# Optimization experiments

Hardware: AMD Instinct MI355X
Metric: run time of the kernel (lower is better)

The kernel has to match this reference:

```python
import jax, jax.numpy as jnp
import numpy as np

BETA = 0.25  # commitment_cost


def setup_inputs() -> dict:
    key = jax.random.key(0)
    k1, k2 = jax.random.split(key)
    N, K, D = 32768, 8192, 512
    z = jax.random.normal(k1, (N, D), dtype=jnp.float32)
    # mimic nn.init.uniform_(codebook, -1/K, 1/K)
    codebook = jax.random.uniform(k2, (K, D), dtype=jnp.float32,
                                  minval=-1.0 / K, maxval=1.0 / K)
    return {"z": z, "codebook": codebook}


def reference(z, codebook):
    # squared L2 distances: ||z||^2 + ||c||^2 - 2 z c^T   -> [N, K]
    d = (jnp.sum(z * z, axis=1, keepdims=True)
         + jnp.sum(codebook * codebook, axis=1)
         - 2.0 * (z @ codebook.T))
    indices = jnp.argmin(d, axis=1)            # [N] int
    z_q = codebook[indices]                    # [N, D] gather (grad flows to codebook)
    # commit_loss = beta * mse(z.detach(), z_q)
    commit_loss = BETA * jnp.mean((jax.lax.stop_gradient(z) - z_q) ** 2)
    # straight-through estimator
    z_st = z + jax.lax.stop_gradient(z_q - z)
    return z_st, indices, commit_loss
```

## Files before the change

kernel.cpp:

```cpp
#include <hip/hip_runtime.h>
#include <cfloat>
#include <cstdint>
#include <cstddef>

#define N_ROWS 32768
#define K_CODES 8192
#define DIM 512
#define BETA 0.25

typedef unsigned short u16;
typedef _Float16 half8 __attribute__((ext_vector_type(8)));
typedef float f32x4 __attribute__((ext_vector_type(4)));

#define BKH 64
#define OVCAP 512
#define DELTA_A 0.4f

#define GLOAD_LDS16(g, l)                                          \
  __builtin_amdgcn_global_load_lds(                                \
      (const __attribute__((address_space(1))) void*)(g),          \
      (__attribute__((address_space(3))) void*)(l), 16, 0, 0)

__device__ inline u16 f2h(float x) {
  union { _Float16 h; u16 u; } c;
  c.h = (_Float16)x;
  return c.u;
}

__global__ __launch_bounds__(256)
void vq_zprep(const float* __restrict__ z, u16* __restrict__ zh,
              float* __restrict__ s1out, int* __restrict__ ovcnt) {
  if (blockIdx.x == 0 && threadIdx.x == 0) *ovcnt = 0;
  const int wv = threadIdx.x >> 6;
  const int lane = threadIdx.x & 63;
  const int half = lane >> 5;
  const int g = (lane >> 3) & 3;
  const int j = lane & 7;
  const int row = blockIdx.x * 8 + wv * 2 + half;
  const float* p = z + (size_t)row * DIM + g * 128 + j;
  u16* q = zh + (size_t)row * DIM + g * 128 + j;
  float x = p[0];
  q[0] = f2h(x);
  float r = __fmul_rn(x, x);
#pragma unroll
  for (int i = 1; i < 16; ++i) {
    x = p[i * 8];
    q[i * 8] = f2h(x);
    r = __fadd_rn(r, __fmul_rn(x, x));
  }
  r = __fadd_rn(r, __shfl_xor(r, 1, 64));
  r = __fadd_rn(r, __shfl_xor(r, 2, 64));
  r = __fadd_rn(r, __shfl_xor(r, 4, 64));
  r = __fadd_rn(r, __shfl_xor(r, 8, 64));
  r = __fadd_rn(r, __shfl_xor(r, 16, 64));
  if ((lane & 31) == 0) s1out[row] = r;
}

__global__ __launch_bounds__(256)
void vq_cvt(const float* __restrict__ src, u16* __restrict__ dst, float scale,
            int n8) {
  int i = blockIdx.x * 256 + threadIdx.x;
  if (i >= n8) return;
  float4 a = ((const float4*)src)[(size_t)i * 2];
  float4 b = ((const float4*)src)[(size_t)i * 2 + 1];
  uint4 o;
  o.x = (unsigned)f2h(a.x * scale) | ((unsigned)f2h(a.y * scale) << 16);
  o.y = (unsigned)f2h(a.z * scale) | ((unsigned)f2h(a.w * scale) << 16);
  o.z = (unsigned)f2h(b.x * scale) | ((unsigned)f2h(b.y * scale) << 16);
  o.w = (unsigned)f2h(b.z * scale) | ((unsigned)f2h(b.w * scale) << 16);
  ((uint4*)dst)[i] = o;
}

__global__ __launch_bounds__(256)
void vq_s1(const float* __restrict__ z, float* __restrict__ s1out) {
  int row = blockIdx.x * 256 + threadIdx.x;
  const float* p = z + (size_t)row * DIM;
  float lf[4];
#pragma unroll
  for (int L = 0; L < 4; ++L) {
    const float* q = p + L * 128;
    float r[8];
#pragma unroll
    for (int j = 0; j < 8; ++j) r[j] = __fmul_rn(q[j], q[j]);
    for (int i = 8; i < 128; i += 8) {
#pragma unroll
      for (int j = 0; j < 8; ++j)
        r[j] = __fadd_rn(r[j], __fmul_rn(q[i + j], q[i + j]));
    }
    float s01 = __fadd_rn(r[0], r[1]);
    float s23 = __fadd_rn(r[2], r[3]);
    float s45 = __fadd_rn(r[4], r[5]);
    float s67 = __fadd_rn(r[6], r[7]);
    lf[L] = __fadd_rn(__fadd_rn(s01, s23), __fadd_rn(s45, s67));
  }
  s1out[row] = __fadd_rn(__fadd_rn(lf[0], lf[1]), __fadd_rn(lf[2], lf[3]));
}

__global__ __launch_bounds__(256, 3)
void vq_gemm(const u16* __restrict__ zh, const u16* __restrict__ ch,
             float* __restrict__ tilemax, uint2* __restrict__ ovlist,
             int* __restrict__ ovcnt, int gcap) {
  __shared__ u16 Ah[128 * BKH];
  __shared__ u16 Bh[128 * BKH];
  __shared__ float rmaxw[2][128];
  __shared__ uint2 obuf[OVCAP];
  __shared__ int ocnt, gbase;
  const int tid = threadIdx.x;
  const int lane = tid & 63;
  const int wid = tid >> 6;
  const int col0 = blockIdx.x * 128;
  const int row0 = blockIdx.y * 128;
  const int wr = (wid >> 1) * 64;
  const int wc = (wid & 1) * 64;
  if (tid == 0) ocnt = 0;

  f32x4 acc[4][4];
#pragma unroll
  for (int m = 0; m < 4; ++m)
#pragma unroll
    for (int n = 0; n < 4; ++n) acc[m][n] = (f32x4){0.f, 0.f, 0.f, 0.f};

  const u16* baseA = zh + (size_t)row0 * DIM;
  const u16* baseB = ch + (size_t)col0 * DIM;
  unsigned offs[4], lofs[4];
#pragma unroll
  for (int jj = 0; jj < 4; ++jj) {
    int p = (wid * 4 + jj) * 1024 + lane * 16;
    int row = p >> 7;
    int ninner = (p & 127) ^ ((row & 7) << 4);
    offs[jj] = (unsigned)(row * DIM + (ninner >> 1));
    lofs[jj] = (wid * 4 + jj) * 512;
  }

  int pbA[4][2], pbB[4][2];
#pragma unroll
  for (int m = 0; m < 4; ++m) {
#pragma unroll
    for (int k2 = 0; k2 < 2; ++k2) {
      int khalf = k2 * 32 + (lane >> 4) * 8;
      int R = wr + m * 16 + (lane & 15);
      pbA[m][k2] = (R * 128 + khalf * 2) ^ ((R & 7) << 4);
      int C = wc + m * 16 + (lane & 15);
      pbB[m][k2] = (C * 128 + khalf * 2) ^ ((C & 7) << 4);
    }
  }

  for (int t = 0; t < DIM / BKH; ++t) {
    __syncthreads();
#pragma unroll
    for (int jj = 0; jj < 4; ++jj) {
      GLOAD_LDS16(baseA + offs[jj] + t * BKH, Ah + lofs[jj]);
      GLOAD_LDS16(baseB + offs[jj] + t * BKH, Bh + lofs[jj]);
    }
    __syncthreads();
#pragma unroll
    for (int k2 = 0; k2 < 2; ++k2) {
      half8 af[4], bf[4];
#pragma unroll
      for (int m = 0; m < 4; ++m)
        af[m] = *(const half8*)((const char*)Ah + pbA[m][k2]);
#pragma unroll
      for (int n = 0; n < 4; ++n)
        bf[n] = *(const half8*)((const char*)Bh + pbB[n][k2]);
#pragma unroll
      for (int m = 0; m < 4; ++m)
#pragma unroll
        for (int n = 0; n < 4; ++n)
          acc[m][n] = __builtin_amdgcn_mfma_f32_16x16x32_f16(af[m], bf[n],
                                                             acc[m][n], 0, 0, 0);
    }
  }

#pragma unroll
  for (int m = 0; m < 4; ++m) {
#pragma unroll
    for (int rg = 0; rg < 4; ++rg) {
      float mx = acc[m][0][rg];
#pragma unroll
      for (int n = 1; n < 4; ++n) mx = fmaxf(mx, acc[m][n][rg]);
#pragma unroll
      for (int s = 1; s <= 8; s <<= 1) mx = fmaxf(mx, __shfl_xor(mx, s, 64));
      int Rloc = wr + m * 16 + (lane >> 4) * 4 + rg;
      if ((lane & 15) == 0) rmaxw[wid & 1][Rloc] = mx;
    }
  }
  __syncthreads();
#pragma unroll
  for (int m = 0; m < 4; ++m) {
#pragma unroll
    for (int rg = 0; rg < 4; ++rg) {
      int Rloc = wr + m * 16 + (lane >> 4) * 4 + rg;
      int grow = row0 + Rloc;
      float gm = fmaxf(rmaxw[0][Rloc], rmaxw[1][Rloc]);
      if ((wid & 1) == 0 && (lane & 15) == 0)
        tilemax[(size_t)blockIdx.x * N_ROWS + grow] = gm;
      float thr = gm - DELTA_A;
#pragma unroll
      for (int n = 0; n < 4; ++n) {
        float v = acc[m][n][rg];
        if (v >= thr) {
          int code = col0 + wc + n * 16 + (lane & 15);
          uint2 e = make_uint2(((unsigned)grow << 13) | (unsigned)code,
                               __float_as_uint(v));
          int p = atomicAdd(&ocnt, 1);
          if (p < OVCAP) obuf[p] = e;
          else {
            int g = atomicAdd(ovcnt, 1);
            if (g < gcap) ovlist[g] = e;
          }
        }
      }
    }
  }
  __syncthreads();
  int n = ocnt < OVCAP ? ocnt : OVCAP;
  if (tid == 0) gbase = atomicAdd(ovcnt, n);
  __syncthreads();
  for (int i = tid; i < n; i += 256) {
    int g = gbase + i;
    if (g < gcap) ovlist[g] = obuf[i];
  }
}

__global__ __launch_bounds__(256)
void vq_merge(const float* __restrict__ tilemax, float* __restrict__ mthr,
              unsigned long long* __restrict__ win) {
  int row = blockIdx.x * 256 + threadIdx.x;
  float g = -1e30f;
  for (int t = 0; t < 64; ++t) g = fmaxf(g, tilemax[(size_t)t * N_ROWS + row]);
  mthr[row] = g - DELTA_A;
  win[row] = ~0ULL;
}

__global__ __launch_bounds__(256)
void vq_init(unsigned long long* __restrict__ win) {
  int row = blockIdx.x * 256 + threadIdx.x;
  win[row] = ~0ULL;
}

__global__ __launch_bounds__(256)
void vq_overflow(const float* __restrict__ z, const float* __restrict__ cb,
                 const float* __restrict__ s1, const float* __restrict__ mthr,
                 const uint2* __restrict__ ovlist, const int* __restrict__ ovcnt,
                 int gcap, unsigned long long* __restrict__ win) {
  int n = *ovcnt;
  if (n > gcap) n = gcap;
  for (int i = blockIdx.x * 256 + threadIdx.x; i < n; i += gridDim.x * 256) {
    uint2 e = ovlist[i];
    int row = e.x >> 13;
    int code = e.x & 8191;
    if (__uint_as_float(e.y) < mthr[row]) continue;
    const float* zp = z + (size_t)row * DIM;
    const float* cp = cb + (size_t)code * DIM;
    float acc = 0.f;
    for (int k = 0; k < DIM; k += 4) {
      float4 zv = *(const float4*)(zp + k);
      float4 cv = *(const float4*)(cp + k);
      acc = fmaf(zv.x, cv.x, acc);
      acc = fmaf(zv.y, cv.y, acc);
      acc = fmaf(zv.z, cv.z, acc);
      acc = fmaf(zv.w, cv.w, acc);
    }
    float dq = __fsub_rn(s1[row], __fmul_rn(2.0f, acc));
    unsigned long long key =
        ((unsigned long long)__float_as_uint(dq) << 32) | (unsigned)code;
    atomicMin(&win[row], key);
  }
}

__global__ __launch_bounds__(256)
void vq_fallback(const float* __restrict__ z, const float* __restrict__ cb,
                 const float* __restrict__ s1, const int* __restrict__ ovcnt,
                 int gcap, int force, unsigned long long* __restrict__ win) {
  if (!force && *ovcnt <= gcap) return;
  __shared__ float zrow[DIM];
  __shared__ unsigned long long red[256];
  for (int row = blockIdx.x; row < N_ROWS; row += gridDim.x) {
    __syncthreads();
    for (int t = threadIdx.x; t < DIM; t += 256) zrow[t] = z[(size_t)row * DIM + t];
    __syncthreads();
    float s1v = s1[row];
    unsigned long long best = ~0ULL;
    for (int j = threadIdx.x; j < K_CODES; j += 256) {
      const float* cp = cb + (size_t)j * DIM;
      float acc = 0.f;
      for (int k = 0; k < DIM; ++k) acc = fmaf(zrow[k], cp[k], acc);
      float dq = __fsub_rn(s1v, __fmul_rn(2.0f, acc));
      unsigned long long key =
          ((unsigned long long)__float_as_uint(dq) << 32) | (unsigned)j;
      if (key < best) best = key;
    }
    red[threadIdx.x] = best;
    __syncthreads();
    for (int s = 128; s > 0; s >>= 1) {
      if (threadIdx.x < s && red[threadIdx.x + s] < red[threadIdx.x])
        red[threadIdx.x] = red[threadIdx.x + s];
      __syncthreads();
    }
    if (threadIdx.x == 0) atomicMin(&win[row], red[0]);
    __syncthreads();
  }
}

__global__ __launch_bounds__(256)
void vq_out(const float* __restrict__ z, const float* __restrict__ cb,
            const unsigned long long* __restrict__ win, float* __restrict__ out,
            double* __restrict__ loss64) {
  int wid = threadIdx.x >> 6, lane = threadIdx.x & 63;
  int row = blockIdx.x * 4 + wid;
  int I1 = (int)(win[row] & 8191ULL);
  const float* zp = z + (size_t)row * DIM + lane * 8;
  const float* cp = cb + (size_t)I1 * DIM + lane * 8;
  float4 z0 = *(const float4*)zp, z1 = *(const float4*)(zp + 4);
  float4 c0 = *(const float4*)cp, c1 = *(const float4*)(cp + 4);
  *(float4*)&out[(size_t)row * DIM + lane * 8] = c0;
  *(float4*)&out[(size_t)row * DIM + lane * 8 + 4] = c1;
  double s = 0.0, d;
  d = (double)z0.x - c0.x; s += d * d;
  d = (double)z0.y - c0.y; s += d * d;
  d = (double)z0.z - c0.z; s += d * d;
  d = (double)z0.w - c0.w; s += d * d;
  d = (double)z1.x - c1.x; s += d * d;
  d = (double)z1.y - c1.y; s += d * d;
  d = (double)z1.z - c1.z; s += d * d;
  d = (double)z1.w - c1.w; s += d * d;
#pragma unroll
  for (int m = 32; m >= 1; m >>= 1) s += __shfl_down(s, m, 64);
  if (lane == 0) {
    loss64[row] = s;
    out[(size_t)N_ROWS * DIM + row] = (float)I1;
  }
}

__global__ __launch_bounds__(1024)
void vq_loss(const double* __restrict__ loss64, float* __restrict__ out) {
  __shared__ double sd[1024];
  double s = 0.0;
  for (int i = threadIdx.x; i < N_ROWS; i += 1024) s += loss64[i];
  sd[threadIdx.x] = s;
  __syncthreads();
  for (int k = 512; k > 0; k >>= 1) {
    if (threadIdx.x < k) sd[threadIdx.x] += sd[threadIdx.x + k];
    __syncthreads();
  }
  if (threadIdx.x == 0)
    out[(size_t)N_ROWS * DIM + N_ROWS] =
        (float)(BETA * sd[0] / ((double)N_ROWS * (double)DIM));
}

extern "C" void kernel_launch(void* const* d_in, const int* in_sizes, int n_in,
                              void* d_out, int out_size, void* d_ws, size_t ws_size,
                              hipStream_t stream) {
  const float* z = (const float*)d_in[0];
  const float* cb = (const float*)d_in[1];
  float* out = (float*)d_out;
  char* ws = (char*)d_ws;

  const size_t OFF_ZH = 0;
  const size_t OFF_CH = 33554432;
  const size_t OFF_S1 = 41943040;
  const size_t OFF_MT = 42074112;
  const size_t OFF_WIN = 42205184;
  const size_t OFF_L64 = 42467328;
  const size_t OFF_TM = 42729472;
  const size_t OFF_OC = 51118080;
  const size_t OFF_OV = 51118096;
  const size_t MIN_FAST = OFF_OV + (size_t)8 * 1024 * 1024;

  if (ws_size >= MIN_FAST) {
    u16* zh = (u16*)(ws + OFF_ZH);
    u16* ch = (u16*)(ws + OFF_CH);
    float* s1f = (float*)(ws + OFF_S1);
    float* mthr = (float*)(ws + OFF_MT);
    unsigned long long* win = (unsigned long long*)(ws + OFF_WIN);
    double* loss64 = (double*)(ws + OFF_L64);
    float* tilemax = (float*)(ws + OFF_TM);
    int* ovcnt = (int*)(ws + OFF_OC);
    uint2* ovlist = (uint2*)(ws + OFF_OV);
    long long gc = (long long)(ws_size - OFF_OV) / 8;
    if (gc > 6 * 1024 * 1024) gc = 6 * 1024 * 1024;
    int gcap = (int)gc;

    vq_zprep<<<N_ROWS / 8, 256, 0, stream>>>(z, zh, s1f, ovcnt);
    vq_cvt<<<K_CODES * DIM / 8 / 256, 256, 0, stream>>>(cb, ch, 4096.0f,
                                                        K_CODES * DIM / 8);
    vq_gemm<<<dim3(K_CODES / 128, N_ROWS / 128), 256, 0, stream>>>(
        zh, ch, tilemax, ovlist, ovcnt, gcap);
    vq_merge<<<N_ROWS / 256, 256, 0, stream>>>(tilemax, mthr, win);
    vq_overflow<<<2048, 256, 0, stream>>>(z, cb, s1f, mthr, ovlist, ovcnt, gcap, win);
    vq_fallback<<<2048, 256, 0, stream>>>(z, cb, s1f, ovcnt, gcap, 0, win);
    vq_out<<<N_ROWS / 4, 256, 0, stream>>>(z, cb, win, out, loss64);
    vq_loss<<<1, 1024, 0, stream>>>(loss64, out);
  } else {
    float* s1f = (float*)(ws + 0);
    unsigned long long* win = (unsigned long long*)(ws + 131072);
    double* loss64 = (double*)(ws + 393216);
    vq_s1<<<N_ROWS / 256, 256, 0, stream>>>(z, s1f);
    vq_init<<<N_ROWS / 256, 256, 0, stream>>>(win);
    vq_fallback<<<2048, 256, 0, stream>>>(z, cb, s1f, nullptr, 0, 1, win);
    vq_out<<<N_ROWS / 4, 256, 0, stream>>>(z, cb, win, out, loss64);
    vq_loss<<<1, 1024, 0, stream>>>(loss64, out);
  }
}
```

Before: 711.4 us.

## Load GEMM A-operand directly from global into registers, vectorize z preprocessing

The GEMM kernel no longer stages the z tile in LDS. Each wave now reads its A fragments straight from global memory into registers, and only the codebook tile still goes through LDS. This halves LDS traffic and footprint, which may raise occupancy, but the A reads become less coalesced (16-byte per lane, strided rows) and are duplicated across the two waves sharing rows. The z-prep kernel is also rewritten to do coalesced float4 loads and half conversion via an LDS staging buffer before the row sum-of-squares reduction.

```diff
diff --git a/kernel.cpp b/kernel.cpp
--- a/kernel.cpp
+++ b/kernel.cpp
@@ -28,24 +28,32 @@
 }
 
 __global__ __launch_bounds__(256)
-void vq_zprep(const float* __restrict__ z, u16* __restrict__ zh,
+void vq_s1lds(const float* __restrict__ z, u16* __restrict__ zh,
               float* __restrict__ s1out, int* __restrict__ ovcnt) {
   if (blockIdx.x == 0 && threadIdx.x == 0) *ovcnt = 0;
-  const int wv = threadIdx.x >> 6;
-  const int lane = threadIdx.x & 63;
-  const int half = lane >> 5;
+  __shared__ float xs[8 * DIM];
+  const int tid = threadIdx.x;
+  const size_t base = (size_t)blockIdx.x * 8 * DIM;
+#pragma unroll
+  for (int c = 0; c < 4; ++c) {
+    int idx = c * 256 + tid;
+    float4 v = ((const float4*)(z + base))[idx];
+    ((float4*)xs)[idx] = v;
+    uint2 h;
+    h.x = (unsigned)f2h(v.x) | ((unsigned)f2h(v.y) << 16);
+    h.y = (unsigned)f2h(v.z) | ((unsigned)f2h(v.w) << 16);
+    ((uint2*)(zh + base))[idx] = h;
+  }
+  __syncthreads();
+  const int lane = tid & 63;
+  const int rowl = tid >> 5;
   const int g = (lane >> 3) & 3;
   const int j = lane & 7;
-  const int row = blockIdx.x * 8 + wv * 2 + half;
-  const float* p = z + (size_t)row * DIM + g * 128 + j;
-  u16* q = zh + (size_t)row * DIM + g * 128 + j;
-  float x = p[0];
-  q[0] = f2h(x);
-  float r = __fmul_rn(x, x);
+  const float* q = xs + rowl * DIM + g * 128 + j;
+  float r = __fmul_rn(q[0], q[0]);
 #pragma unroll
   for (int i = 1; i < 16; ++i) {
-    x = p[i * 8];
-    q[i * 8] = f2h(x);
+    float x = q[i * 8];
     r = __fadd_rn(r, __fmul_rn(x, x));
   }
   r = __fadd_rn(r, __shfl_xor(r, 1, 64));
@@ -53,7 +61,7 @@
   r = __fadd_rn(r, __shfl_xor(r, 4, 64));
   r = __fadd_rn(r, __shfl_xor(r, 8, 64));
   r = __fadd_rn(r, __shfl_xor(r, 16, 64));
-  if ((lane & 31) == 0) s1out[row] = r;
+  if ((lane & 31) == 0) s1out[blockIdx.x * 8 + rowl] = r;
 }
 
 __global__ __launch_bounds__(256)
@@ -100,7 +108,6 @@
 void vq_gemm(const u16* __restrict__ zh, const u16* __restrict__ ch,
              float* __restrict__ tilemax, uint2* __restrict__ ovlist,
              int* __restrict__ ovcnt, int gcap) {
-  __shared__ u16 Ah[128 * BKH];
   __shared__ u16 Bh[128 * BKH];
   __shared__ float rmaxw[2][128];
   __shared__ uint2 obuf[OVCAP];
@@ -120,45 +127,46 @@
 #pragma unroll
     for (int n = 0; n < 4; ++n) acc[m][n] = (f32x4){0.f, 0.f, 0.f, 0.f};
 
-  const u16* baseA = zh + (size_t)row0 * DIM;
   const u16* baseB = ch + (size_t)col0 * DIM;
-  unsigned offs[4], lofs[4];
+  unsigned offsB[4], lofsB[4];
 #pragma unroll
   for (int jj = 0; jj < 4; ++jj) {
     int p = (wid * 4 + jj) * 1024 + lane * 16;
     int row = p >> 7;
     int ninner = (p & 127) ^ ((row & 7) << 4);
-    offs[jj] = (unsigned)(row * DIM + (ninner >> 1));
-    lofs[jj] = (wid * 4 + jj) * 512;
-  }
-
-  int pbA[4][2], pbB[4][2];
-#pragma unroll
-  for (int m = 0; m < 4; ++m) {
+    offsB[jj] = (unsigned)(row * DIM + (ninner >> 1));
+    lofsB[jj] = (wid * 4 + jj) * 512;
+  }
+
+  const u16* pA = zh + (size_t)(row0 + wr + (lane & 15)) * DIM + (lane >> 4) * 8;
+
+  int pbB[4][2];
+#pragma unroll
+  for (int n = 0; n < 4; ++n) {
 #pragma unroll
     for (int k2 = 0; k2 < 2; ++k2) {
       int khalf = k2 * 32 + (lane >> 4) * 8;
-      int R = wr + m * 16 + (lane & 15);
-      pbA[m][k2] = (R * 128 + khalf * 2) ^ ((R & 7) << 4);
-      int C = wc + m * 16 + (lane & 15);
-      pbB[m][k2] = (C * 128 + khalf * 2) ^ ((C & 7) << 4);
+      int C = wc + n * 16 + (lane & 15);
+      pbB[n][k2] = (C * 128 + khalf * 2) ^ ((C & 7) << 4);
     }
   }
 
   for (int t = 0; t < DIM / BKH; ++t) {
     __syncthreads();
 #pragma unroll
-    for (int jj = 0; jj < 4; ++jj) {
-      GLOAD_LDS16(baseA + offs[jj] + t * BKH, Ah + lofs[jj]);
-      GLOAD_LDS16(baseB + offs[jj] + t * BKH, Bh + lofs[jj]);
-    }
+    for (int jj = 0; jj < 4; ++jj)
+      GLOAD_LDS16(baseB + offsB[jj] + t * BKH, Bh + lofsB[jj]);
+    half8 af[4][2];
+#pragma unroll
+    for (int m = 0; m < 4; ++m)
+#pragma unroll
+      for (int k2 = 0; k2 < 2; ++k2)
+        af[m][k2] = *(const half8*)(pA + m * 16 * DIM + t * BKH + k2 * 32);
+    __builtin_amdgcn_sched_barrier(0);
     __syncthreads();
 #pragma unroll
     for (int k2 = 0; k2 < 2; ++k2) {
-      half8 af[4], bf[4];
-#pragma unroll
-      for (int m = 0; m < 4; ++m)
-        af[m] = *(const half8*)((const char*)Ah + pbA[m][k2]);
+      half8 bf[4];
 #pragma unroll
       for (int n = 0; n < 4; ++n)
         bf[n] = *(const half8*)((const char*)Bh + pbB[n][k2]);
@@ -166,7 +174,7 @@
       for (int m = 0; m < 4; ++m)
 #pragma unroll
         for (int n = 0; n < 4; ++n)
-          acc[m][n] = __builtin_amdgcn_mfma_f32_16x16x32_f16(af[m], bf[n],
+          acc[m][n] = __builtin_amdgcn_mfma_f32_16x16x32_f16(af[m][k2], bf[n],
                                                              acc[m][n], 0, 0, 0);
     }
   }
@@ -381,7 +389,7 @@
     if (gc > 6 * 1024 * 1024) gc = 6 * 1024 * 1024;
     int gcap = (int)gc;
 
-    vq_zprep<<<N_ROWS / 8, 256, 0, stream>>>(z, zh, s1f, ovcnt);
+    vq_s1lds<<<N_ROWS / 8, 256, 0, stream>>>(z, zh, s1f, ovcnt);
     vq_cvt<<<K_CODES * DIM / 8 / 256, 256, 0, stream>>>(cb, ch, 4096.0f,
                                                         K_CODES * DIM / 8);
     vq_gemm<<<dim3(K_CODES / 128, N_ROWS / 128), 256, 0, stream>>>(
```

After: 867.5 us. 21.9% more time.
